# Kernel optimization log

Measured on AMD Instinct MI355X. Metric: run time of the kernel, lower is better.

The kernel has to match this reference:

```python
import jax, jax.numpy as jnp
import numpy as np

# MoE config (matches init_kwargs)
DMODEL = 1024
N_EXPERTS = 32
EXPERT_SIZE = 512
N_HEADS = 4  # top-k experts per token
WEIGHT_SCALE = 1.0


def setup_inputs() -> dict:
    key = jax.random.key(0)
    k0, k1, k2, k3 = jax.random.split(key, 4)
    x = jax.random.normal(k0, (2, 2048, DMODEL), dtype=jnp.float32)
    # expert selection keys: [n_experts, dmodel], std = dmodel**-0.5
    expert_sel = jax.random.normal(k1, (N_EXPERTS, DMODEL), dtype=jnp.float32) * (DMODEL ** -0.5)
    # expert input keys: [n_experts, dmodel, expert_size], std = dmodel**-0.5
    keys = jax.random.normal(k2, (N_EXPERTS, DMODEL, EXPERT_SIZE), dtype=jnp.float32) * (DMODEL ** -0.5)
    # expert output values: [n_experts, expert_size, v_dim], std = (n_experts*expert_size)**-0.5
    values = jax.random.normal(k3, (N_EXPERTS, EXPERT_SIZE, DMODEL), dtype=jnp.float32) * ((N_EXPERTS * EXPERT_SIZE) ** -0.5)
    return {"x": x, "expert_sel": expert_sel, "keys": keys, "values": values}


def reference(x, expert_sel, keys, values):
    # x: [B, S, D]
    B, S, D = x.shape
    xt = x.reshape(-1, D)                      # [N, D] tokens
    N = xt.shape[0]

    # --- routing: sigmoid gating + top-k expert selection ---
    sel_logits = jnp.einsum('nd,ed->ne', xt, expert_sel)   # [N, E]
    gates = jax.nn.sigmoid(sel_logits)                     # [N, E]
    sel_val, sel_idx = jax.lax.top_k(gates, N_HEADS)       # [N, K]

    # scatter selected gate values into a dense [N, E] gate matrix
    # (zero gate for non-selected experts == gather/scatter of expert MLPs)
    gate_full = jnp.zeros_like(gates).at[jnp.arange(N)[:, None], sel_idx].set(sel_val)

    # --- expert MLP: key scores -> ReLU -> gate-weighted -> value combine ---
    scores = jax.nn.relu(jnp.einsum('nd,edf->nef', xt, keys))   # [N, E, F]
    scores = scores * gate_full[:, :, None]                     # mask + sigmoid gate
    out = jnp.einsum('nef,efv->nv', scores, values)             # [N, V]

    return out.reshape(B, S, -1)
```

## Files before the change

kernel.cpp:

```cpp
#include <hip/hip_runtime.h>

#define DMODEL 1024
#define NEXP   32
#define FDIM   512
#define TOPK   4

#define MT1   256
#define MT2   128
#define BK    64
#define RTB   8
#define NBORD 64

using short8 = __attribute__((ext_vector_type(8))) short;
using f32x4  = __attribute__((ext_vector_type(4))) float;

#define AS1 __attribute__((address_space(1)))
#define AS3 __attribute__((address_space(3)))
__device__ __forceinline__ void gload_lds16(const void* g, void* l) {
    __builtin_amdgcn_global_load_lds((const AS1 unsigned int*)g, (AS3 unsigned int*)l, 16, 0, 0);
}

__device__ __forceinline__ unsigned short f2b(float f) {
    unsigned int u = __float_as_uint(f);
    unsigned int r = (u + 0x7FFFu + ((u >> 16) & 1u)) >> 16;
    return (unsigned short)r;
}
__device__ __forceinline__ float b2f(unsigned short u) {
    return __uint_as_float((unsigned int)u << 16);
}

__device__ __forceinline__ int xcd_swz(int bid, int nwg) {
    int q = nwg >> 3, r = nwg & 7;
    int xcd = bid & 7, sub = bid >> 3;
    return (xcd < r ? xcd * (q + 1) : r * (q + 1) + (xcd - r) * q) + sub;
}

__global__ __launch_bounds__(256) void route_a(
    const float* __restrict__ x, const float* __restrict__ esel,
    unsigned short* __restrict__ xb,
    unsigned int* __restrict__ sel_e, float* __restrict__ sel_g, int ntok)
{
    int tile0 = blockIdx.x * RTB;
    int tid = threadIdx.x;

    __shared__ float xs[RTB][DMODEL];
    __shared__ float gs[RTB][NEXP];

    {
        const float4* src = (const float4*)(x + (size_t)tile0 * DMODEL);
        float4* dst = (float4*)&xs[0][0];
        int navail = min(RTB, ntok - tile0) * (DMODEL / 4);
        for (int i = tid; i < RTB * (DMODEL / 4); i += 256)
            dst[i] = src[i < navail ? i : 0];
    }
    __syncthreads();

    int e = tid >> 3, sub = tid & 7;
    float4 acc0 = {0,0,0,0}, acc1 = {0,0,0,0}, acc2 = {0,0,0,0}, acc3 = {0,0,0,0};
    float4 acc4 = {0,0,0,0}, acc5 = {0,0,0,0}, acc6 = {0,0,0,0}, acc7 = {0,0,0,0};
    const float* er = esel + (size_t)e * DMODEL + sub * 4;
    #pragma unroll 4
    for (int j = 0; j < DMODEL / 32; j++) {
        float4 ev = *(const float4*)(er + j * 32);
        int kk = sub * 4 + j * 32;
        float4 x0 = *(const float4*)(&xs[0][kk]);
        float4 x1 = *(const float4*)(&xs[1][kk]);
        float4 x2 = *(const float4*)(&xs[2][kk]);
        float4 x3 = *(const float4*)(&xs[3][kk]);
        float4 x4 = *(const float4*)(&xs[4][kk]);
        float4 x5 = *(const float4*)(&xs[5][kk]);
        float4 x6 = *(const float4*)(&xs[6][kk]);
        float4 x7 = *(const float4*)(&xs[7][kk]);
        acc0.x += ev.x*x0.x; acc0.y += ev.y*x0.y; acc0.z += ev.z*x0.z; acc0.w += ev.w*x0.w;
        acc1.x += ev.x*x1.x; acc1.y += ev.y*x1.y; acc1.z += ev.z*x1.z; acc1.w += ev.w*x1.w;
        acc2.x += ev.x*x2.x; acc2.y += ev.y*x2.y; acc2.z += ev.z*x2.z; acc2.w += ev.w*x2.w;
        acc3.x += ev.x*x3.x; acc3.y += ev.y*x3.y; acc3.z += ev.z*x3.z; acc3.w += ev.w*x3.w;
        acc4.x += ev.x*x4.x; acc4.y += ev.y*x4.y; acc4.z += ev.z*x4.z; acc4.w += ev.w*x4.w;
        acc5.x += ev.x*x5.x; acc5.y += ev.y*x5.y; acc5.z += ev.z*x5.z; acc5.w += ev.w*x5.w;
        acc6.x += ev.x*x6.x; acc6.y += ev.y*x6.y; acc6.z += ev.z*x6.z; acc6.w += ev.w*x6.w;
        acc7.x += ev.x*x7.x; acc7.y += ev.y*x7.y; acc7.z += ev.z*x7.z; acc7.w += ev.w*x7.w;
    }
    {
        float s[RTB] = {
            acc0.x+acc0.y+acc0.z+acc0.w, acc1.x+acc1.y+acc1.z+acc1.w,
            acc2.x+acc2.y+acc2.z+acc2.w, acc3.x+acc3.y+acc3.z+acc3.w,
            acc4.x+acc4.y+acc4.z+acc4.w, acc5.x+acc5.y+acc5.z+acc5.w,
            acc6.x+acc6.y+acc6.z+acc6.w, acc7.x+acc7.y+acc7.z+acc7.w };
        #pragma unroll
        for (int t = 0; t < RTB; t++) {
            float v = s[t];
            v += __shfl_xor(v, 1);
            v += __shfl_xor(v, 2);
            v += __shfl_xor(v, 4);
            if (sub == 0) gs[t][e] = 1.f / (1.f + expf(-v));
        }
    }
    __syncthreads();

    {
        int t = tid >> 5, e2 = tid & 31;
        int tok = tile0 + t;
        if (tok < ntok) {
            float v = gs[t][e2];
            #pragma unroll
            for (int r = 0; r < TOPK; r++) {
                float bv = v; int bi = e2;
                #pragma unroll
                for (int sft = 16; sft >= 1; sft >>= 1) {
                    float ov = __shfl_xor(bv, sft, 32);
                    int   oi = __shfl_xor(bi, sft, 32);
                    if (ov > bv || (ov == bv && oi < bi)) { bv = ov; bi = oi; }
                }
                if (e2 == bi) v = -1e30f;
                if (e2 == r) {
                    sel_e[(size_t)tok * TOPK + r] = (unsigned)bi;
                    sel_g[(size_t)tok * TOPK + r] = bv;
                }
            }
        }
    }

    {
        int navail = min(RTB, ntok - tile0) * (DMODEL / 4);
        ushort4* dst = (ushort4*)(xb + (size_t)tile0 * DMODEL);
        const float4* srcl = (const float4*)&xs[0][0];
        for (int i = tid; i < navail; i += 256) {
            float4 v = srcl[i];
            ushort4 o;
            o.x = f2b(v.x); o.y = f2b(v.y); o.z = f2b(v.z); o.w = f2b(v.w);
            dst[i] = o;
        }
    }
}

__global__ __launch_bounds__(256) void hist_k(
    const unsigned int* __restrict__ sel_e, int* __restrict__ ghist, int nsel)
{
    __shared__ int h[NEXP];
    int tid = threadIdx.x;
    if (tid < NEXP) h[tid] = 0;
    __syncthreads();
    int chunk = (nsel + gridDim.x - 1) / gridDim.x;
    int i0 = blockIdx.x * chunk, i1 = min(i0 + chunk, nsel);
    for (int i = i0 + tid; i < i1; i += 256)
        atomicAdd(&h[sel_e[i]], 1);
    __syncthreads();
    if (tid < NEXP) ghist[blockIdx.x * NEXP + tid] = h[tid];
}

__global__ __launch_bounds__(64) void scan2_k(
    const int* __restrict__ ghist, int* __restrict__ goff,
    int* __restrict__ counts, int* __restrict__ base,
    int* __restrict__ tiles1, int* __restrict__ tiles2,
    int* __restrict__ ntiles, int nb)
{
    int e = threadIdx.x;
    if (e < NEXP) {
        int s = 0;
        for (int b = 0; b < nb; b++) {
            goff[b * NEXP + e] = s;
            s += ghist[b * NEXP + e];
        }
        counts[e] = s;
    }
    __syncthreads();
    if (e == 0) {
        int s = 0, nt1 = 0, nt2 = 0;
        for (int e2 = 0; e2 < NEXP; e2++) {
            base[e2] = s;
            int c = counts[e2];
            for (int t0 = 0; t0 < c; t0 += MT1) tiles1[nt1++] = (e2 << 8) | (t0 / MT1);
            for (int t0 = 0; t0 < c; t0 += MT2) tiles2[nt2++] = (e2 << 8) | (t0 / MT2);
            s += c;
        }
        ntiles[0] = nt1;
        ntiles[1] = nt2;
    }
}

__global__ __launch_bounds__(256) void scat_k(
    const unsigned int* __restrict__ sel_e, const float* __restrict__ sel_g,
    const int* __restrict__ goff,
    int* __restrict__ tok_list, float* __restrict__ gate_list,
    unsigned int* __restrict__ slotinfo, int nsel, int ntok)
{
    __shared__ int c[NEXP];
    int tid = threadIdx.x;
    if (tid < NEXP) c[tid] = goff[blockIdx.x * NEXP + tid];
    __syncthreads();
    int chunk = (nsel + gridDim.x - 1) / gridDim.x;
    int i0 = blockIdx.x * chunk, i1 = min(i0 + chunk, nsel);
    for (int i = i0 + tid; i < i1; i += 256) {
        unsigned int e = sel_e[i];
        float g = sel_g[i];
        int pos = atomicAdd(&c[e], 1);
        tok_list [(size_t)e * ntok + pos] = i >> 2;
        gate_list[(size_t)e * ntok + pos] = g;
        slotinfo[i] = (e << 16) | (unsigned)pos;
    }
}

__global__ __launch_bounds__(256) void prep_t(const float* __restrict__ src,
                                              unsigned short* __restrict__ dst,
                                              int R, int C) {
    __shared__ float tile[64][65];
    int e  = blockIdx.z;
    int r0 = blockIdx.y * 64, c0 = blockIdx.x * 64;
    const float* s = src + (size_t)e * R * C;
    unsigned short* d = dst + (size_t)e * R * C;
    for (int i = 0; i < 16; i++) {
        int c = i * 256 + threadIdx.x;
        int rr = c >> 6, cc = c & 63;
        tile[rr][cc] = s[(size_t)(r0 + rr) * C + c0 + cc];
    }
    __syncthreads();
    for (int i = 0; i < 16; i++) {
        int c = i * 256 + threadIdx.x;
        int wr = c >> 6, wc = c & 63;
        d[(size_t)(c0 + wr) * R + r0 + wc] = f2b(tile[wc][wr]);
    }
}

__global__ __launch_bounds__(512, 2) void gemm1_k(
    const unsigned short* __restrict__ xb,
    const unsigned short* __restrict__ kt,
    const int* __restrict__ counts, const int* __restrict__ base,
    const int* __restrict__ tiles, const int* __restrict__ ntiles,
    const int* __restrict__ tok_list, const float* __restrict__ gate_list,
    unsigned short* __restrict__ hs, int ntok)
{
    int flat = xcd_swz(blockIdx.x, gridDim.x);
    int ti = flat >> 1;
    int f0 = (flat & 1) << 8;
    if (ti >= ntiles[0]) return;
    int code = tiles[ti];
    int e = code >> 8, t0 = (code & 255) * MT1;
    int cnt  = counts[e];
    int live = min(MT1, cnt - t0);

    __shared__ unsigned short Xs[2][MT1 * BK];
    __shared__ unsigned short Ks[2][256 * BK];
    __shared__ int   toks[MT1];
    __shared__ float gts[MT1];

    int tid = threadIdx.x, lane = tid & 63, wid = tid >> 6;
    int wr = wid >> 2, wc = wid & 3;
    int lr = lane & 15, lg = lane >> 4;

    if (tid < MT1) {
        bool lv = tid < live;
        toks[tid] = lv ? tok_list [(size_t)e * ntok + t0 + tid] : 0;
        gts[tid]  = lv ? gate_list[(size_t)e * ntok + t0 + tid] : 0.f;
    }
    __syncthreads();

    int lrow = lane >> 3;
    int scol = ((lane & 7) ^ lrow) * 8;
    const unsigned short* ke = kt + (size_t)e * FDIM * DMODEL + (size_t)f0 * DMODEL;
    const unsigned short* sx[4];
    const unsigned short* sk[4];
    int dofs[4];
    #pragma unroll
    for (int j = 0; j < 4; j++) {
        int ch = 4 * wid + j;
        int row = ch * 8 + lrow;
        sx[j] = xb + (size_t)toks[row] * DMODEL + scol;
        sk[j] = ke + (size_t)row * DMODEL + scol;
        dofs[j] = ch * 512;
    }

    f32x4 acc[8][4];
    #pragma unroll
    for (int m = 0; m < 8; m++)
        #pragma unroll
        for (int n = 0; n < 4; n++)
            acc[m][n] = (f32x4){0.f, 0.f, 0.f, 0.f};

    #pragma unroll
    for (int j = 0; j < 4; j++) {
        gload_lds16(sx[j], &Xs[0][dofs[j]]);
        gload_lds16(sk[j], &Ks[0][dofs[j]]);
    }

    int cur = 0;
    const int NKT = DMODEL / BK;
    for (int t = 0; t < NKT; t++) {
        bool more = (t + 1) < NKT;
        if (more) {
            int k1 = (t + 1) * BK;
            #pragma unroll
            for (int j = 0; j < 4; j++) {
                gload_lds16(sx[j] + k1, &Xs[cur ^ 1][dofs[j]]);
                gload_lds16(sk[j] + k1, &Ks[cur ^ 1][dofs[j]]);
            }
            asm volatile("s_waitcnt vmcnt(8)" ::: "memory");
        } else {
            asm volatile("s_waitcnt vmcnt(0)" ::: "memory");
        }
        __builtin_amdgcn_s_barrier();
        __builtin_amdgcn_sched_barrier(0);
        const unsigned short* Xc = Xs[cur];
        const unsigned short* Kc = Ks[cur];
        #pragma unroll
        for (int ks = 0; ks < 2; ks++) {
            short8 a[8];
            #pragma unroll
            for (int m = 0; m < 8; m++) {
                int row = wr * 128 + m * 16 + lr;
                a[m] = *(const short8*)(Xc + row * BK + (((ks * 4 + lg) ^ (lr & 7)) * 8));
            }
            #pragma unroll
            for (int n = 0; n < 4; n++) {
                int row = wc * 64 + n * 16 + lr;
                short8 b = *(const short8*)(Kc + row * BK + (((ks * 4 + lg) ^ (lr & 7)) * 8));
                #pragma unroll
                for (int m = 0; m < 8; m++)
                    acc[m][n] = __builtin_amdgcn_mfma_f32_16x16x32_bf16(a[m], b, acc[m][n], 0, 0, 0);
            }
        }
        __builtin_amdgcn_sched_barrier(0);
        asm volatile("s_waitcnt lgkmcnt(0)" ::: "memory");
        __builtin_amdgcn_s_barrier();
        cur ^= 1;
    }

    int hb = base[e] + t0;
    #pragma unroll
    for (int m = 0; m < 8; m++) {
        #pragma unroll
        for (int n = 0; n < 4; n++) {
            int col = f0 + wc * 64 + n * 16 + lr;
            #pragma unroll
            for (int r = 0; r < 4; r++) {
                int row = wr * 128 + m * 16 + lg * 4 + r;
                if (row < live)
                    hs[(size_t)(hb + row) * FDIM + col] = f2b(fmaxf(acc[m][n][r], 0.f) * gts[row]);
            }
        }
    }
}

__global__ __launch_bounds__(256) void gemm2_k(
    const unsigned short* __restrict__ hs,
    const unsigned short* __restrict__ vt,
    const int* __restrict__ counts, const int* __restrict__ base,
    const int* __restrict__ tiles2, const int* __restrict__ ntiles,
    unsigned short* __restrict__ ys)
{
    int flat = xcd_swz(blockIdx.x, gridDim.x);
    int ti = flat >> 3;
    int v0 = (flat & 7) << 7;
    if (ti >= ntiles[1]) return;
    int code = tiles2[ti];
    int e = code >> 8, t0 = (code & 255) * MT2;
    int cnt  = counts[e];
    int live = min(MT2, cnt - t0);
    int hb   = base[e] + t0;

    __shared__ unsigned short Hs[2][MT2 * BK];
    __shared__ unsigned short Vs[2][128 * BK];

    int tid = threadIdx.x, lane = tid & 63, w = tid >> 6;
    int lr = lane & 15, lg = lane >> 4;

    int lrow = lane >> 3;
    int scol = ((lane & 7) ^ lrow) * 8;
    const unsigned short* he = hs + (size_t)hb * FDIM;
    const unsigned short* ve = vt + (size_t)e * DMODEL * FDIM + (size_t)v0 * FDIM;
    const unsigned short* sh[4];
    const unsigned short* sv[4];
    int dofs[4];
    #pragma unroll
    for (int j = 0; j < 4; j++) {
        int ch = 4 * w + j;
        int row = ch * 8 + lrow;
        sh[j] = he + (size_t)row * FDIM + scol;
        sv[j] = ve + (size_t)row * FDIM + scol;
        dofs[j] = ch * 512;
    }

    f32x4 acc[8][2];
    #pragma unroll
    for (int m = 0; m < 8; m++)
        #pragma unroll
        for (int n = 0; n < 2; n++)
            acc[m][n] = (f32x4){0.f, 0.f, 0.f, 0.f};

    #pragma unroll
    for (int j = 0; j < 4; j++) {
        gload_lds16(sh[j], &Hs[0][dofs[j]]);
        gload_lds16(sv[j], &Vs[0][dofs[j]]);
    }

    int cur = 0;
    const int NKT = FDIM / BK;
    for (int t = 0; t < NKT; t++) {
        bool more = (t + 1) < NKT;
        if (more) {
            int k1 = (t + 1) * BK;
            #pragma unroll
            for (int j = 0; j < 4; j++) {
                gload_lds16(sh[j] + k1, &Hs[cur ^ 1][dofs[j]]);
                gload_lds16(sv[j] + k1, &Vs[cur ^ 1][dofs[j]]);
            }
            asm volatile("s_waitcnt vmcnt(8)" ::: "memory");
        } else {
            asm volatile("s_waitcnt vmcnt(0)" ::: "memory");
        }
        __builtin_amdgcn_s_barrier();
        __builtin_amdgcn_sched_barrier(0);
        const unsigned short* Hc = Hs[cur];
        const unsigned short* Vc = Vs[cur];
        #pragma unroll
        for (int ks = 0; ks < 2; ks++) {
            short8 a[8];
            #pragma unroll
            for (int m = 0; m < 8; m++) {
                int row = m * 16 + lr;
                a[m] = *(const short8*)(Hc + row * BK + (((ks * 4 + lg) ^ (lr & 7)) * 8));
            }
            #pragma unroll
            for (int n = 0; n < 2; n++) {
                int row = w * 32 + n * 16 + lr;
                short8 b = *(const short8*)(Vc + row * BK + (((ks * 4 + lg) ^ (lr & 7)) * 8));
                #pragma unroll
                for (int m = 0; m < 8; m++)
                    acc[m][n] = __builtin_amdgcn_mfma_f32_16x16x32_bf16(a[m], b, acc[m][n], 0, 0, 0);
            }
        }
        __builtin_amdgcn_sched_barrier(0);
        asm volatile("s_waitcnt lgkmcnt(0)" ::: "memory");
        __builtin_amdgcn_s_barrier();
        cur ^= 1;
    }

    #pragma unroll
    for (int m = 0; m < 8; m++) {
        #pragma unroll
        for (int n = 0; n < 2; n++) {
            int col = v0 + w * 32 + n * 16 + lr;
            #pragma unroll
            for (int r = 0; r < 4; r++) {
                int row = m * 16 + lg * 4 + r;
                if (row < live)
                    ys[(size_t)(hb + row) * DMODEL + col] = f2b(acc[m][n][r]);
            }
        }
    }
}

__global__ __launch_bounds__(256) void combine_k(
    const unsigned short* __restrict__ ys, const unsigned int* __restrict__ slotinfo,
    const int* __restrict__ base, float* __restrict__ out)
{
    int tok = blockIdx.x;
    unsigned int s0 = slotinfo[(size_t)tok * TOPK + 0];
    unsigned int s1 = slotinfo[(size_t)tok * TOPK + 1];
    unsigned int s2 = slotinfo[(size_t)tok * TOPK + 2];
    unsigned int s3 = slotinfo[(size_t)tok * TOPK + 3];
    const ushort4* y0 = (const ushort4*)(ys + (size_t)(base[s0 >> 16] + (s0 & 0xFFFF)) * DMODEL);
    const ushort4* y1 = (const ushort4*)(ys + (size_t)(base[s1 >> 16] + (s1 & 0xFFFF)) * DMODEL);
    const ushort4* y2 = (const ushort4*)(ys + (size_t)(base[s2 >> 16] + (s2 & 0xFFFF)) * DMODEL);
    const ushort4* y3 = (const ushort4*)(ys + (size_t)(base[s3 >> 16] + (s3 & 0xFFFF)) * DMODEL);
    int i = threadIdx.x;
    ushort4 a = y0[i], b = y1[i], c = y2[i], d = y3[i];
    float4 o;
    o.x = b2f(a.x) + b2f(b.x) + b2f(c.x) + b2f(d.x);
    o.y = b2f(a.y) + b2f(b.y) + b2f(c.y) + b2f(d.y);
    o.z = b2f(a.z) + b2f(b.z) + b2f(c.z) + b2f(d.z);
    o.w = b2f(a.w) + b2f(b.w) + b2f(c.w) + b2f(d.w);
    ((float4*)(out + (size_t)tok * DMODEL))[i] = o;
}

#define BTF 16
__global__ __launch_bounds__(256) void expert_k(
    const float* __restrict__ x, const float* __restrict__ keys,
    const float* __restrict__ values, const int* __restrict__ counts,
    const int* __restrict__ tok_list, const float* __restrict__ gate_list,
    float* __restrict__ out, int ntok)
{
    int e   = blockIdx.y;
    int cnt = counts[e];
    int t0  = blockIdx.x * BTF;
    if (t0 >= cnt) return;
    int nt = (cnt - t0 < BTF) ? (cnt - t0) : BTF;

    __shared__ float xs[BTF][DMODEL];
    __shared__ float hsl[BTF][FDIM];
    __shared__ int   toks[BTF];
    __shared__ float gts[BTF];

    if (threadIdx.x < BTF) {
        int t = threadIdx.x;
        bool live = (t < nt);
        toks[t] = live ? tok_list [(size_t)e * ntok + t0 + t] : 0;
        gts[t]  = live ? gate_list[(size_t)e * ntok + t0 + t] : 0.f;
    }
    __syncthreads();
    for (int i = threadIdx.x; i < BTF * (DMODEL / 4); i += 256) {
        int r = i >> 8, c = i & 255;
        ((float4*)xs[r])[c] = ((const float4*)(x + (size_t)toks[r] * DMODEL))[c];
    }
    __syncthreads();

    {
        int f = threadIdx.x * 2;
        float acc0[BTF], acc1[BTF];
        #pragma unroll
        for (int t = 0; t < BTF; t++) { acc0[t] = 0.f; acc1[t] = 0.f; }
        const float* kp = keys + (size_t)e * DMODEL * FDIM + f;
        for (int k = 0; k < DMODEL; k += 4) {
            const float* kr = kp + (size_t)k * FDIM;
            float2 kv0 = *(const float2*)(kr);
            float2 kv1 = *(const float2*)(kr + FDIM);
            float2 kv2 = *(const float2*)(kr + 2 * FDIM);
            float2 kv3 = *(const float2*)(kr + 3 * FDIM);
            #pragma unroll
            for (int t = 0; t < BTF; t++) {
                float4 xv = *(const float4*)(&xs[t][k]);
                acc0[t] += xv.x * kv0.x + xv.y * kv1.x + xv.z * kv2.x + xv.w * kv3.x;
                acc1[t] += xv.x * kv0.y + xv.y * kv1.y + xv.z * kv2.y + xv.w * kv3.y;
            }
        }
        #pragma unroll
        for (int t = 0; t < BTF; t++) {
            float g = gts[t];
            hsl[t][f]     = fmaxf(acc0[t], 0.f) * g;
            hsl[t][f + 1] = fmaxf(acc1[t], 0.f) * g;
        }
    }
    __syncthreads();

    {
        int v = threadIdx.x * 4;
        float acc[BTF][4];
        #pragma unroll
        for (int t = 0; t < BTF; t++) { acc[t][0]=0.f; acc[t][1]=0.f; acc[t][2]=0.f; acc[t][3]=0.f; }
        const float* vp = values + (size_t)e * FDIM * DMODEL + v;
        for (int k = 0; k < FDIM; k += 2) {
            float4 va0 = *(const float4*)(vp + (size_t)k * DMODEL);
            float4 va1 = *(const float4*)(vp + (size_t)(k + 1) * DMODEL);
            #pragma unroll
            for (int t = 0; t < BTF; t++) {
                float2 hv = *(const float2*)(&hsl[t][k]);
                acc[t][0] += hv.x * va0.x + hv.y * va1.x;
                acc[t][1] += hv.x * va0.y + hv.y * va1.y;
                acc[t][2] += hv.x * va0.z + hv.y * va1.z;
                acc[t][3] += hv.x * va0.w + hv.y * va1.w;
            }
        }
        #pragma unroll
        for (int t = 0; t < BTF; t++) {
            if (t < nt) {
                float* orow = out + (size_t)toks[t] * DMODEL + v;
                atomicAdd(orow + 0, acc[t][0]);
                atomicAdd(orow + 1, acc[t][1]);
                atomicAdd(orow + 2, acc[t][2]);
                atomicAdd(orow + 3, acc[t][3]);
            }
        }
    }
}

extern "C" void kernel_launch(void* const* d_in, const int* in_sizes, int n_in,
                              void* d_out, int out_size, void* d_ws, size_t ws_size,
                              hipStream_t stream) {
    const float* x      = (const float*)d_in[0];
    const float* esel   = (const float*)d_in[1];
    const float* keys   = (const float*)d_in[2];
    const float* values = (const float*)d_in[3];
    float* out = (float*)d_out;
    int ntok = in_sizes[0] / DMODEL;

    const size_t OFF_BASE  = 512;
    const size_t OFF_NT    = 1024;
    const size_t OFF_TILE1 = 2048;
    const size_t OFF_TILE2 = 8 << 10;
    const size_t OFF_HIST  = 16 << 10;
    const size_t OFF_GOFF  = 32 << 10;
    const size_t OFF_SLOT  = 64 << 10;
    const size_t OFF_SELE  = 128 << 10;
    const size_t OFF_SELG  = 192 << 10;
    const size_t OFF_TOK   = 256 << 10;
    const size_t OFF_GATE  = 1ull << 20;
    const size_t OFF_XB    = 2ull << 20;
    const size_t OFF_KT    = 12ull << 20;
    const size_t OFF_VT    = 46ull << 20;
    const size_t OFF_HS    = 80ull << 20;
    const size_t OFF_YS    = 98ull << 20;
    const size_t NEED      = OFF_YS + (size_t)ntok * TOPK * DMODEL * sizeof(float) + (1 << 20);

    int*      counts    = (int*)d_ws;
    int*      ebase     = (int*)((char*)d_ws + OFF_BASE);
    int*      ntiles    = (int*)((char*)d_ws + OFF_NT);
    int*      tiles1    = (int*)((char*)d_ws + OFF_TILE1);
    int*      tiles2    = (int*)((char*)d_ws + OFF_TILE2);
    int*      ghist     = (int*)((char*)d_ws + OFF_HIST);
    int*      goff      = (int*)((char*)d_ws + OFF_GOFF);
    unsigned* slotinfo  = (unsigned*)((char*)d_ws + OFF_SLOT);
    unsigned* sel_e     = (unsigned*)((char*)d_ws + OFF_SELE);
    float*    sel_g     = (float*)((char*)d_ws + OFF_SELG);
    int*      tok_list  = (int*)((char*)d_ws + OFF_TOK);
    float*    gate_list = (float*)((char*)d_ws + OFF_GATE);
    unsigned short* xb  = (unsigned short*)((char*)d_ws + OFF_XB);

    int nsel = ntok * TOPK;
    int rblocks = (ntok + RTB - 1) / RTB;
    route_a<<<rblocks, 256, 0, stream>>>(x, esel, xb, sel_e, sel_g, ntok);
    hist_k<<<NBORD, 256, 0, stream>>>(sel_e, ghist, nsel);
    scan2_k<<<1, 64, 0, stream>>>(ghist, goff, counts, ebase, tiles1, tiles2,
                                  ntiles, NBORD);
    scat_k<<<NBORD, 256, 0, stream>>>(sel_e, sel_g, goff, tok_list, gate_list,
                                      slotinfo, nsel, ntok);

    if (ws_size >= NEED) {
        unsigned short* kt = (unsigned short*)((char*)d_ws + OFF_KT);
        unsigned short* vt = (unsigned short*)((char*)d_ws + OFF_VT);
        unsigned short* hs = (unsigned short*)((char*)d_ws + OFF_HS);
        unsigned short* ys = (unsigned short*)((char*)d_ws + OFF_YS);

        prep_t<<<dim3(FDIM / 64, DMODEL / 64, NEXP), 256, 0, stream>>>(keys,   kt, DMODEL, FDIM);
        prep_t<<<dim3(DMODEL / 64, FDIM / 64, NEXP), 256, 0, stream>>>(values, vt, FDIM, DMODEL);

        int maxt1 = (nsel + MT1 - 1) / MT1 + NEXP;
        int maxt2 = (nsel + MT2 - 1) / MT2 + NEXP;
        gemm1_k<<<dim3(maxt1 * (FDIM / 256)), 512, 0, stream>>>(
            xb, kt, counts, ebase, tiles1, ntiles, tok_list, gate_list, hs, ntok);
        gemm2_k<<<dim3(maxt2 * (DMODEL / 128)), 256, 0, stream>>>(
            hs, vt, counts, ebase, tiles2, ntiles, ys);
        combine_k<<<ntok, 256, 0, stream>>>(ys, slotinfo, ebase, out);
    } else {
        hipMemsetAsync(out, 0, (size_t)out_size * sizeof(float), stream);
        int ntiles2f = (ntok + BTF - 1) / BTF;
        expert_k<<<dim3(ntiles2f, NEXP), 256, 0, stream>>>(
            x, keys, values, counts, tok_list, gate_list, out, ntok);
    }
}
```

Before: 193.8 us.

## Shrink gemm1 N tile to 128 and add triple-buffered LDS prefetch

Gemm1 now splits the expert F dimension into four 128-wide tiles instead of two 256-wide ones. This doubles the block count and halves per-wave accumulators. The K loop becomes a three-stage LDS pipeline with two tiles in flight, using adjusted vmcnt waits. The aim is more parallelism and better latency hiding, at the cost of re-reading the gathered X rows twice as often and lower MFMA reuse per block.

```diff
diff --git a/kernel.cpp b/kernel.cpp
--- a/kernel.cpp
+++ b/kernel.cpp
@@ -6,6 +6,7 @@
 #define TOPK   4
 
 #define MT1   256
+#define NT1   128
 #define MT2   128
 #define BK    64
 #define RTB   8
@@ -230,21 +231,21 @@
     unsigned short* __restrict__ hs, int ntok)
 {
     int flat = xcd_swz(blockIdx.x, gridDim.x);
-    int ti = flat >> 1;
-    int f0 = (flat & 1) << 8;
+    int ti = flat >> 2;
+    int f0 = (flat & 3) << 7;
     if (ti >= ntiles[0]) return;
     int code = tiles[ti];
     int e = code >> 8, t0 = (code & 255) * MT1;
     int cnt  = counts[e];
     int live = min(MT1, cnt - t0);
 
-    __shared__ unsigned short Xs[2][MT1 * BK];
-    __shared__ unsigned short Ks[2][256 * BK];
+    __shared__ unsigned short Xs[3][MT1 * BK];
+    __shared__ unsigned short Ks[3][NT1 * BK];
     __shared__ int   toks[MT1];
     __shared__ float gts[MT1];
 
     int tid = threadIdx.x, lane = tid & 63, wid = tid >> 6;
-    int wr = wid >> 2, wc = wid & 3;
+    int wr = wid >> 1, wc = wid & 1;
     int lr = lane & 15, lg = lane >> 4;
 
     if (tid < MT1) {
@@ -258,55 +259,64 @@
     int scol = ((lane & 7) ^ lrow) * 8;
     const unsigned short* ke = kt + (size_t)e * FDIM * DMODEL + (size_t)f0 * DMODEL;
     const unsigned short* sx[4];
-    const unsigned short* sk[4];
-    int dofs[4];
+    const unsigned short* sk[2];
+    int dox[4], dok[2];
     #pragma unroll
     for (int j = 0; j < 4; j++) {
         int ch = 4 * wid + j;
         int row = ch * 8 + lrow;
         sx[j] = xb + (size_t)toks[row] * DMODEL + scol;
+        dox[j] = ch * 512;
+    }
+    #pragma unroll
+    for (int j = 0; j < 2; j++) {
+        int ch = 2 * wid + j;
+        int row = ch * 8 + lrow;
         sk[j] = ke + (size_t)row * DMODEL + scol;
-        dofs[j] = ch * 512;
-    }
-
-    f32x4 acc[8][4];
-    #pragma unroll
-    for (int m = 0; m < 8; m++)
+        dok[j] = ch * 512;
+    }
+
+    f32x4 acc[4][4];
+    #pragma unroll
+    for (int m = 0; m < 4; m++)
         #pragma unroll
         for (int n = 0; n < 4; n++)
             acc[m][n] = (f32x4){0.f, 0.f, 0.f, 0.f};
 
     #pragma unroll
-    for (int j = 0; j < 4; j++) {
-        gload_lds16(sx[j], &Xs[0][dofs[j]]);
-        gload_lds16(sk[j], &Ks[0][dofs[j]]);
-    }
-
-    int cur = 0;
+    for (int tt = 0; tt < 2; tt++) {
+        int kk = tt * BK;
+        #pragma unroll
+        for (int j = 0; j < 4; j++) gload_lds16(sx[j] + kk, &Xs[tt][dox[j]]);
+        #pragma unroll
+        for (int j = 0; j < 2; j++) gload_lds16(sk[j] + kk, &Ks[tt][dok[j]]);
+    }
+
     const int NKT = DMODEL / BK;
     for (int t = 0; t < NKT; t++) {
-        bool more = (t + 1) < NKT;
-        if (more) {
-            int k1 = (t + 1) * BK;
-            #pragma unroll
-            for (int j = 0; j < 4; j++) {
-                gload_lds16(sx[j] + k1, &Xs[cur ^ 1][dofs[j]]);
-                gload_lds16(sk[j] + k1, &Ks[cur ^ 1][dofs[j]]);
-            }
-            asm volatile("s_waitcnt vmcnt(8)" ::: "memory");
+        if (t + 2 < NKT) {
+            int k2 = (t + 2) * BK;
+            int b2 = (t + 2) % 3;
+            #pragma unroll
+            for (int j = 0; j < 4; j++) gload_lds16(sx[j] + k2, &Xs[b2][dox[j]]);
+            #pragma unroll
+            for (int j = 0; j < 2; j++) gload_lds16(sk[j] + k2, &Ks[b2][dok[j]]);
+            asm volatile("s_waitcnt vmcnt(12)" ::: "memory");
+        } else if (t + 1 < NKT) {
+            asm volatile("s_waitcnt vmcnt(6)" ::: "memory");
         } else {
             asm volatile("s_waitcnt vmcnt(0)" ::: "memory");
         }
         __builtin_amdgcn_s_barrier();
         __builtin_amdgcn_sched_barrier(0);
-        const unsigned short* Xc = Xs[cur];
-        const unsigned short* Kc = Ks[cur];
+        const unsigned short* Xc = Xs[t % 3];
+        const unsigned short* Kc = Ks[t % 3];
         #pragma unroll
         for (int ks = 0; ks < 2; ks++) {
-            short8 a[8];
-            #pragma unroll
-            for (int m = 0; m < 8; m++) {
-                int row = wr * 128 + m * 16 + lr;
+            short8 a[4];
+            #pragma unroll
+            for (int m = 0; m < 4; m++) {
+                int row = wr * 64 + m * 16 + lr;
                 a[m] = *(const short8*)(Xc + row * BK + (((ks * 4 + lg) ^ (lr & 7)) * 8));
             }
             #pragma unroll
@@ -314,25 +324,24 @@
                 int row = wc * 64 + n * 16 + lr;
                 short8 b = *(const short8*)(Kc + row * BK + (((ks * 4 + lg) ^ (lr & 7)) * 8));
                 #pragma unroll
-                for (int m = 0; m < 8; m++)
+                for (int m = 0; m < 4; m++)
                     acc[m][n] = __builtin_amdgcn_mfma_f32_16x16x32_bf16(a[m], b, acc[m][n], 0, 0, 0);
             }
         }
         __builtin_amdgcn_sched_barrier(0);
         asm volatile("s_waitcnt lgkmcnt(0)" ::: "memory");
         __builtin_amdgcn_s_barrier();
-        cur ^= 1;
     }
 
     int hb = base[e] + t0;
     #pragma unroll
-    for (int m = 0; m < 8; m++) {
+    for (int m = 0; m < 4; m++) {
         #pragma unroll
         for (int n = 0; n < 4; n++) {
             int col = f0 + wc * 64 + n * 16 + lr;
             #pragma unroll
             for (int r = 0; r < 4; r++) {
-                int row = wr * 128 + m * 16 + lg * 4 + r;
+                int row = wr * 64 + m * 16 + lg * 4 + r;
                 if (row < live)
                     hs[(size_t)(hb + row) * FDIM + col] = f2b(fmaxf(acc[m][n][r], 0.f) * gts[row]);
             }
@@ -624,7 +633,7 @@
 
         int maxt1 = (nsel + MT1 - 1) / MT1 + NEXP;
         int maxt2 = (nsel + MT2 - 1) / MT2 + NEXP;
-        gemm1_k<<<dim3(maxt1 * (FDIM / 256)), 512, 0, stream>>>(
+        gemm1_k<<<dim3(maxt1 * (FDIM / NT1)), 512, 0, stream>>>(
             xb, kt, counts, ebase, tiles1, ntiles, tok_list, gate_list, hs, ntok);
         gemm2_k<<<dim3(maxt2 * (DMODEL / 128)), 256, 0, stream>>>(
             hs, vt, counts, ebase, tiles2, ntiles, ys);
```

After: 190.5 us. Within noise of the previous version (-1.7%).
